# Kernel tuning notes

Hardware: AMD Instinct MI355X
Metric: run time of the kernel (lower is better)

## Reference

```python
import jax, jax.numpy as jnp
import numpy as np

# Config matching init_kwargs: input_shape=(C,T,H,W)=(512,32,14,14), window_size=9, n_heads=8
B, C, T, H, W = 2, 512, 32, 14, 14
N, K = 8, 9
CI = C // N              # per-head inter channels (64)
P = (K - 1) // 2         # symmetric temporal zero-pad so S == T


def setup_inputs() -> dict:
    key = jax.random.key(0)
    ks = jax.random.split(key, 7)
    s = 0.02
    return {
        "x":  jax.random.normal(ks[0], (B, C, T, H, W), jnp.float32),
        # per-head 1x1x1 conv (Linear3d) weights/biases, stacked over heads
        "Wq": jax.random.normal(ks[1], (N, CI, C), jnp.float32) * s,
        "bq": jax.random.normal(ks[2], (N, CI), jnp.float32) * s,
        "Wk": jax.random.normal(ks[3], (N, CI, C), jnp.float32) * s,
        "bk": jax.random.normal(ks[4], (N, CI), jnp.float32) * s,
        "Wv": jax.random.normal(ks[5], (N, CI, C), jnp.float32) * s,
        "bv": jax.random.normal(ks[6], (N, CI), jnp.float32) * s,
    }


def reference(x, Wq, bq, Wk, bk, Wv, bv):
    # x: (B, C, T, H, W). Dropout (p=0.25) is inference-mode identity.
    Bx, Cx, Tx, Hx, Wd = x.shape
    HW = Hx * Wd
    xf = x.reshape(Bx, Cx, Tx, HW)

    # Queries: every original frame is the center of its own window -> project x directly.
    q = jnp.einsum('bctp,nic->bnitp', xf, Wq) + bq[None, :, :, None, None]  # (B,N,ci,T,HW)

    # Keys/values on temporally zero-padded input (Pad3d gives S == T windows).
    xp = jnp.pad(xf, ((0, 0), (0, 0), (P, P), (0, 0)))  # (B,C,T+K-1,HW)
    k = jnp.einsum('bctp,nic->bnitp', xp, Wk) + bk[None, :, :, None, None]
    v = jnp.einsum('bctp,nic->bnitp', xp, Wv) + bv[None, :, :, None, None]

    # Sliding windows over padded time: window s covers padded frames s..s+K-1
    win = jnp.arange(Tx)[:, None] + jnp.arange(K)[None, :]  # (T,K)
    kw = k[:, :, :, win]  # (B,N,ci,T,K,HW)
    vw = v[:, :, :, win].reshape(Bx, N, CI, Tx, K * HW)

    # alpha[b,n,t,p,m] = sum_i q[b,n,i,t,p] * k_win[b,n,i,t,m]; softmax over keys m
    alpha = jnp.einsum('bnitp,bnitkm->bntpkm', q, kw).reshape(Bx, N, Tx, HW, K * HW)
    alpha = jax.nn.softmax(alpha, axis=-1)

    # y = alpha @ value -> (B,N,ci,T,HW); head concat is channel-major reshape
    y = jnp.einsum('bntpm,bnitm->bnitp', alpha, vw)
    z = y.reshape(Bx, Cx, Tx, Hx, Wd) + x  # residual
    return z
```

## Files before the change

### kernel.cpp

```cpp
#include <hip/hip_runtime.h>
#include <hip/hip_bf16.h>
#include <stdint.h>
#include <cstddef>

#define BB  2
#define CC  512
#define TT  32
#define HWP 196
#define NH  8
#define KWIN 9
#define CID 64
#define PPAD 4
#define TP  40
#define MTOT 12544
#define NTOT 1536
#define VSLOT 224
#define LOG2E 1.44269504f

typedef unsigned short u16;
typedef unsigned int   u32;
typedef __attribute__((ext_vector_type(8))) short short8;
typedef __attribute__((ext_vector_type(4))) float floatx4;

__device__ __forceinline__ u16 f2bf(float f) {
    u32 u = __float_as_uint(f);
    u32 r = (u + 0x7fffu + ((u >> 16) & 1u)) >> 16;
    return (u16)r;
}
__device__ __forceinline__ u32 pack2bf(float a, float b) {
    return (u32)f2bf(a) | ((u32)f2bf(b) << 16);
}
__device__ __forceinline__ u32 packtrunc(float a, float b) {
    return __builtin_amdgcn_perm(__float_as_uint(b), __float_as_uint(a), 0x07060302u);
}
__device__ __forceinline__ float fexp2(float x) {
    return __builtin_amdgcn_exp2f(x);
}
__device__ __forceinline__ void gload16(const u16* g, u16* l) {
    __builtin_amdgcn_global_load_lds(
        (const __attribute__((address_space(1))) u32*)g,
        (__attribute__((address_space(3))) u32*)l, 16, 0, 0);
}

__global__ __launch_bounds__(256) void prep_transpose(
    const float* __restrict__ x, u16* __restrict__ xt,
    const float* __restrict__ Wq, const float* __restrict__ Wk,
    const float* __restrict__ Wv, u16* __restrict__ Wbf,
    const float* __restrict__ bk, const float* __restrict__ bv,
    u16* __restrict__ Kout, u16* __restrict__ Vtp)
{
    __shared__ float T[64 * 197];
    int bxg = blockIdx.x;
    int tid = threadIdx.x;

    if (bxg < BB * TT * 8) {
        int bx = bxg;
        int ct = bx & 7; bx >>= 3;
        int t = bx & 31;
        int b = bx >> 5;
        const float* src = x + ((size_t)(b * CC + ct * 64) * TT + t) * HWP;
        for (int i = tid; i < 64 * 49; i += 256) {
            int c = i / 49;
            int p4 = i - c * 49;
            float4 v = *(const float4*)(src + (size_t)c * (TT * HWP) + p4 * 4);
            float* Tp = &T[c * 197 + p4 * 4];
            Tp[0] = v.x; Tp[1] = v.y; Tp[2] = v.z; Tp[3] = v.w;
        }
        __syncthreads();
        u16* dst = xt + (size_t)((b * TT + t) * HWP) * CC + ct * 64;
        for (int i = tid; i < HWP * 8; i += 256) {
            int p = i >> 3;
            int c0 = (i & 7) * 8;
            u32 w[4];
            #pragma unroll
            for (int k = 0; k < 4; k++)
                w[k] = pack2bf(T[(c0 + 2 * k) * 197 + p],
                               T[(c0 + 2 * k + 1) * 197 + p]);
            *(uint4*)(dst + (size_t)p * CC + c0) = *(uint4*)w;
        }
        return;
    }

    int id = (bxg - BB * TT * 8) * 256 + tid;
    const int wtot = NTOT * CC / 2;
    const int kper = 2 * NH * 8 * HWP * 32;
    const int vper = 2 * NH * 8 * 64 * (VSLOT/2);
    if (id < wtot) {
        int c2 = id & 255;
        int oc = id >> 8;
        int kind = oc >> 9;
        int idx = oc & 511;
        const float* src = (kind == 0 ? Wq : (kind == 1 ? Wk : Wv)) + (size_t)idx * CC + c2 * 2;
        ((u32*)Wbf)[id] = pack2bf(src[0], src[1]);
    } else if (id < wtot + kper) {
        int i = id - wtot;
        int ci2 = i & 31; i >>= 5;
        int p = i % HWP;  i /= HWP;
        int fr = i & 7;   i >>= 3;
        int head = i & 7;
        int b = i >> 3;
        int tp = fr < 4 ? fr : fr + 32;
        const float* bias = bk + head * CID + ci2 * 2;
        size_t addr = (((size_t)(b * NH + head) * TP + tp) * HWP + p) * 32 + ci2;
        ((u32*)Kout)[addr] = pack2bf(bias[0], bias[1]);
    } else if (id < wtot + kper + vper) {
        int i = id - wtot - kper;
        int s2 = i % (VSLOT/2); i /= (VSLOT/2);
        int ci = i & 63; i >>= 6;
        int fr = i & 7;  i >>= 3;
        int head = i & 7;
        int b = i >> 3;
        int tp = fr < 4 ? fr : fr + 32;
        float bias = bv[head * CID + ci];
        size_t addr = (((size_t)(b * NH + head) * TP + tp) * 64 + ci) * (VSLOT/2) + s2;
        ((u32*)Vtp)[addr] = pack2bf(bias, bias);
    }
}

__global__ __launch_bounds__(512) void proj_gemm2(
    const u16* __restrict__ xt, const u16* __restrict__ Wbf,
    const float* __restrict__ bq, const float* __restrict__ bk,
    const float* __restrict__ bv,
    u16* __restrict__ Qout, u16* __restrict__ Kout, u16* __restrict__ Vtp)
{
    __shared__ u16 sA[128 * 64];
    __shared__ u16 sB[256 * 64];

    int bx = blockIdx.x;
    int nb = bx % 6;
    int mt = bx / 6;
    int tid = threadIdx.x;
    int wave = tid >> 6, lane = tid & 63, quad = lane >> 4, l15 = lane & 15;
    int wm = wave >> 2, wn = wave & 3;
    int mbase = mt * 128 + wm * 64;
    int nbase = nb * 256 + wn * 64;

    int lr = lane >> 3;
    int sw = ((lane & 7) * 8) ^ (lr << 3);

    floatx4 acc[4][4];
    #pragma unroll
    for (int ms = 0; ms < 4; ms++)
        #pragma unroll
        for (int ns = 0; ns < 4; ns++)
            acc[ms][ns] = (floatx4){0.f, 0.f, 0.f, 0.f};

    const u16* abase = xt + (size_t)(mt * 128) * CC;
    const u16* bbase = Wbf + (size_t)(nb * 256) * CC;

    for (int kc = 0; kc < 8; kc++) {
        __syncthreads();
        #pragma unroll
        for (int i = 0; i < 2; i++) {
            int rbase = wave * 16 + i * 8;
            gload16(abase + (size_t)(rbase + lr) * CC + kc * 64 + sw,
                    &sA[rbase * 64]);
        }
        #pragma unroll
        for (int i = 0; i < 4; i++) {
            int rbase = wave * 32 + i * 8;
            gload16(bbase + (size_t)(rbase + lr) * CC + kc * 64 + sw,
                    &sB[rbase * 64]);
        }
        __syncthreads();

        #pragma unroll
        for (int kk = 0; kk < 2; kk++) {
            int swr = (kk * 32 + quad * 8) ^ ((l15 & 7) << 3);
            short8 af[4], bf[4];
            #pragma unroll
            for (int ms = 0; ms < 4; ms++)
                af[ms] = *(const short8*)&sA[(wm * 64 + ms * 16 + l15) * 64 + swr];
            #pragma unroll
            for (int ns = 0; ns < 4; ns++)
                bf[ns] = *(const short8*)&sB[(wn * 64 + ns * 16 + l15) * 64 + swr];
            #pragma unroll
            for (int ms = 0; ms < 4; ms++)
                #pragma unroll
                for (int ns = 0; ns < 4; ns++)
                    acc[ms][ns] = __builtin_amdgcn_mfma_f32_16x16x32_bf16(
                        af[ms], bf[ns], acc[ms][ns], 0, 0, 0);
        }
    }

    float biasv[4];
    #pragma unroll
    for (int ns = 0; ns < 4; ns++) {
        int n = nbase + ns * 16 + l15;
        int kind = n >> 9;
        int idx = n & 511;
        const float* bpb = kind == 0 ? bq : (kind == 1 ? bk : bv);
        biasv[ns] = bpb[idx];
    }

    #pragma unroll
    for (int ms = 0; ms < 4; ms++) {
        #pragma unroll
        for (int r = 0; r < 4; r++) {
            int m = mbase + ms * 16 + quad * 4 + r;
            int b = m / (TT * HWP);
            int rem = m - b * (TT * HWP);
            int t = rem / HWP;
            int p = rem - t * HWP;
            int slot_p = (p & ~31) | (p & 3) | (((p >> 4) & 1) << 2)
                       | (((p >> 2) & 1) << 3) | (((p >> 3) & 1) << 4);
            #pragma unroll
            for (int ns = 0; ns < 4; ns++) {
                int n = nbase + ns * 16 + l15;
                int kind = n >> 9;
                int idx = n & 511;
                int head = idx >> 6;
                int ci = idx & 63;
                float val = acc[ms][ns][r] + biasv[ns];
                if (kind == 0) {
                    Qout[(((size_t)(b * NH + head) * TT + t) * HWP + p) * CID + ci]
                        = f2bf(val * LOG2E);
                } else if (kind == 1) {
                    Kout[(((size_t)(b * NH + head) * TP + (t + PPAD)) * HWP + p) * CID + ci]
                        = f2bf(val);
                } else {
                    Vtp[(((size_t)(b * NH + head) * TP + (t + PPAD)) * 64 + ci) * VSLOT + slot_p]
                        = f2bf(val);
                }
            }
        }
    }
}

__global__ __launch_bounds__(256, 1) void attn_mfma4(
    const float* __restrict__ x,
    const u16* __restrict__ Qb, const u16* __restrict__ Kb,
    const u16* __restrict__ Vtp, float* __restrict__ zout)
{
    __shared__ float eT[192 * 66];
    __shared__ float eT12[4][4][66];
    __shared__ float ls12[4][4];

    int i = blockIdx.x;
    int xcd = i & 7;
    int r = i >> 3;
    int slab = ((r >= 32) ? 8 : 0) | xcd;
    int t = r & 31;
    int b = slab >> 3, n = slab & 7;

    int tid = threadIdx.x;
    int wave = tid >> 6;
    int lane = tid & 63;
    int quad = lane >> 4, l15 = lane & 15;

    const u16* kfr0 = Kb + (size_t)slab * (TP * HWP) * CID;
    const u16* vslab = Vtp + (size_t)slab * (TP * 64 * VSLOT);
    const float tmask = (quad == 0) ? 1.0f : 0.0f;

    short8 qf[3][2];
    #pragma unroll
    for (int j = 0; j < 3; j++) {
        int qrow = (wave + 4 * j) * 16 + l15;
        const u16* qp = Qb + ((size_t)(slab * TT + t) * HWP + qrow) * CID;
        qf[j][0] = *(const short8*)(qp + quad * 8);
        qf[j][1] = *(const short8*)(qp + 32 + quad * 8);
    }
    short8 qf12[2];
    {
        int qrow = 192 + l15;
        qrow = qrow < HWP ? qrow : (HWP - 1);
        const u16* qp = Qb + ((size_t)(slab * TT + t) * HWP + qrow) * CID;
        qf12[0] = *(const short8*)(qp + quad * 8);
        qf12[1] = *(const short8*)(qp + 32 + quad * 8);
    }

    floatx4 acc[3][4];
    floatx4 accl[3];
    floatx4 acc12[4];
    floatx4 accl12;
    #pragma unroll
    for (int j = 0; j < 3; j++) {
        #pragma unroll
        for (int cg = 0; cg < 4; cg++) acc[j][cg] = (floatx4){0.f, 0.f, 0.f, 0.f};
        accl[j] = (floatx4){0.f, 0.f, 0.f, 0.f};
    }
    #pragma unroll
    for (int cg = 0; cg < 4; cg++) acc12[cg] = (floatx4){0.f, 0.f, 0.f, 0.f};
    accl12 = (floatx4){0.f, 0.f, 0.f, 0.f};

    union { u32 w[4]; short8 s; } ones;
    ones.w[0] = 0x3F803F80u; ones.w[1] = 0x3F803F80u;
    ones.w[2] = 0x3F803F80u; ones.w[3] = 0x3F803F80u;

    #define KLOAD(c, D00, D01, D10, D11) do {                                    \
        const u16* a0_ = kfr0 + (size_t)(rbase + (c) * 32 + l15) * CID + quad * 8;\
        const u16* a1_ = a0_ + (size_t)16 * CID;                                 \
        D00 = *(const short8*)a0_;  D01 = *(const short8*)(a0_ + 32);            \
        D10 = *(const short8*)a1_;  D11 = *(const short8*)(a1_ + 32);            \
    } while (0)

    #define KLOADTAIL(D00, D01) do {                                             \
        int g_ = rbase + 192 + l15;                                              \
        g_ = g_ < (TP * HWP - 1) ? g_ : (TP * HWP - 1);                          \
        const u16* a0_ = kfr0 + (size_t)g_ * CID + quad * 8;                     \
        D00 = *(const short8*)a0_;  D01 = *(const short8*)(a0_ + 32);            \
    } while (0)

    #define VLOAD(c, D0, D1, D2, D3) do {                                        \
        const u16* v_ = vfr + l15 * VSLOT + (c) * 32 + quad * 8;                 \
        D0 = *(const short8*)v_;                                                 \
        D1 = *(const short8*)(v_ + 16 * VSLOT);                                  \
        D2 = *(const short8*)(v_ + 32 * VSLOT);                                  \
        D3 = *(const short8*)(v_ + 48 * VSLOT);                                  \
    } while (0)

    #define CHUNK_ONE(Q0, Q1, ACC, ACCL, K00, K01, K10, K11, V0, V1, V2, V3) do {\
        floatx4 sc0 = (floatx4){0.f, 0.f, 0.f, 0.f};                             \
        sc0 = __builtin_amdgcn_mfma_f32_16x16x32_bf16(K00, Q0, sc0, 0, 0, 0);    \
        sc0 = __builtin_amdgcn_mfma_f32_16x16x32_bf16(K01, Q1, sc0, 0, 0, 0);    \
        floatx4 sc1 = (floatx4){0.f, 0.f, 0.f, 0.f};                             \
        sc1 = __builtin_amdgcn_mfma_f32_16x16x32_bf16(K10, Q0, sc1, 0, 0, 0);    \
        sc1 = __builtin_amdgcn_mfma_f32_16x16x32_bf16(K11, Q1, sc1, 0, 0, 0);    \
        union { u32 w[4]; short8 s; } pf;                                        \
        pf.w[0] = packtrunc(fexp2(sc0[0]), fexp2(sc0[1]));                       \
        pf.w[1] = packtrunc(fexp2(sc0[2]), fexp2(sc0[3]));                       \
        pf.w[2] = packtrunc(fexp2(sc1[0]), fexp2(sc1[1]));                       \
        pf.w[3] = packtrunc(fexp2(sc1[2]), fexp2(sc1[3]));                       \
        ACC[0] = __builtin_amdgcn_mfma_f32_16x16x32_bf16(pf.s, V0, ACC[0], 0, 0, 0); \
        ACC[1] = __builtin_amdgcn_mfma_f32_16x16x32_bf16(pf.s, V1, ACC[1], 0, 0, 0); \
        ACC[2] = __builtin_amdgcn_mfma_f32_16x16x32_bf16(pf.s, V2, ACC[2], 0, 0, 0); \
        ACC[3] = __builtin_amdgcn_mfma_f32_16x16x32_bf16(pf.s, V3, ACC[3], 0, 0, 0); \
        ACCL   = __builtin_amdgcn_mfma_f32_16x16x32_bf16(pf.s, ones.s, ACCL, 0, 0, 0); \
    } while (0)

    #define TAIL_ONE(Q0, Q1, ACC, ACCL, K00, K01, V0, V1, V2, V3) do {           \
        floatx4 sc0 = (floatx4){0.f, 0.f, 0.f, 0.f};                             \
        sc0 = __builtin_amdgcn_mfma_f32_16x16x32_bf16(K00, Q0, sc0, 0, 0, 0);    \
        sc0 = __builtin_amdgcn_mfma_f32_16x16x32_bf16(K01, Q1, sc0, 0, 0, 0);    \
        union { u32 w[4]; short8 s; } pf;                                        \
        pf.w[0] = packtrunc(fexp2(sc0[0]) * tmask, fexp2(sc0[1]) * tmask);       \
        pf.w[1] = packtrunc(fexp2(sc0[2]) * tmask, fexp2(sc0[3]) * tmask);       \
        pf.w[2] = 0u;                                                            \
        pf.w[3] = 0u;                                                            \
        ACC[0] = __builtin_amdgcn_mfma_f32_16x16x32_bf16(pf.s, V0, ACC[0], 0, 0, 0); \
        ACC[1] = __builtin_amdgcn_mfma_f32_16x16x32_bf16(pf.s, V1, ACC[1], 0, 0, 0); \
        ACC[2] = __builtin_amdgcn_mfma_f32_16x16x32_bf16(pf.s, V2, ACC[2], 0, 0, 0); \
        ACC[3] = __builtin_amdgcn_mfma_f32_16x16x32_bf16(pf.s, V3, ACC[3], 0, 0, 0); \
        ACCL   = __builtin_amdgcn_mfma_f32_16x16x32_bf16(pf.s, ones.s, ACCL, 0, 0, 0); \
    } while (0)

    #define CHUNK_FULL(K00, K01, K10, K11, V0, V1, V2, V3) do {                  \
        _Pragma("unroll")                                                        \
        for (int j = 0; j < 3; j++)                                              \
            CHUNK_ONE(qf[j][0], qf[j][1], acc[j], accl[j],                       \
                      K00, K01, K10, K11, V0, V1, V2, V3);                       \
        if (do12)                                                                \
            CHUNK_ONE(qf12[0], qf12[1], acc12, accl12,                           \
                      K00, K01, K10, K11, V0, V1, V2, V3);                       \
    } while (0)

    #define CHUNK_TAIL(K00, K01, V0, V1, V2, V3) do {                            \
        _Pragma("unroll")                                                        \
        for (int j = 0; j < 3; j++)                                              \
            TAIL_ONE(qf[j][0], qf[j][1], acc[j], accl[j],                        \
                     K00, K01, V0, V1, V2, V3);                                  \
        if (do12)                                                                \
            TAIL_ONE(qf12[0], qf12[1], acc12, accl12,                            \
                     K00, K01, V0, V1, V2, V3);                                  \
    } while (0)

    for (int f = 0; f < KWIN; f++) {
        int rbase = (t + f) * HWP;
        const u16* vfr = vslab + (size_t)(t + f) * (64 * VSLOT);
        bool do12 = ((f & 3) == wave);

        short8 ka00, ka01, ka10, ka11, va0, va1, va2, va3;
        short8 kb00, kb01, kb10, kb11, vb0, vb1, vb2, vb3;
        short8 kc00, kc01, kc10, kc11, vc0, vc1, vc2, vc3;

        KLOAD(0, ka00, ka01, ka10, ka11);  VLOAD(0, va0, va1, va2, va3);
        KLOAD(1, kb00, kb01, kb10, kb11);  VLOAD(1, vb0, vb1, vb2, vb3);
        KLOAD(2, kc00, kc01, kc10, kc11);  VLOAD(2, vc0, vc1, vc2, vc3);
        CHUNK_FULL(ka00, ka01, ka10, ka11, va0, va1, va2, va3);
        KLOAD(3, ka00, ka01, ka10, ka11);  VLOAD(3, va0, va1, va2, va3);
        CHUNK_FULL(kb00, kb01, kb10, kb11, vb0, vb1, vb2, vb3);
        KLOAD(4, kb00, kb01, kb10, kb11);  VLOAD(4, vb0, vb1, vb2, vb3);
        CHUNK_FULL(kc00, kc01, kc10, kc11, vc0, vc1, vc2, vc3);
        KLOAD(5, kc00, kc01, kc10, kc11);  VLOAD(5, vc0, vc1, vc2, vc3);
        CHUNK_FULL(ka00, ka01, ka10, ka11, va0, va1, va2, va3);
        KLOADTAIL(ka00, ka01);             VLOAD(6, va0, va1, va2, va3);
        CHUNK_FULL(kb00, kb01, kb10, kb11, vb0, vb1, vb2, vb3);
        CHUNK_FULL(kc00, kc01, kc10, kc11, vc0, vc1, vc2, vc3);
        CHUNK_TAIL(ka00, ka01, va0, va1, va2, va3);
    }

    #undef KLOAD
    #undef KLOADTAIL
    #undef VLOAD
    #undef CHUNK_ONE
    #undef TAIL_ONE
    #undef CHUNK_FULL
    #undef CHUNK_TAIL

    #pragma unroll
    for (int j = 0; j < 3; j++) {
        int tg = wave + 4 * j;
        float il[4];
        #pragma unroll
        for (int rr = 0; rr < 4; rr++) il[rr] = 1.0f / accl[j][rr];
        #pragma unroll
        for (int cg = 0; cg < 4; cg++) {
            #pragma unroll
            for (int rr = 0; rr < 4; rr++) {
                int p = tg * 16 + quad * 4 + rr;
                eT[p * 66 + cg * 16 + l15] = acc[j][cg][rr] * il[rr];
            }
        }
    }
    if (quad == 0) {
        #pragma unroll
        for (int rr = 0; rr < 4; rr++) {
            #pragma unroll
            for (int cg = 0; cg < 4; cg++)
                eT12[wave][rr][cg * 16 + l15] = acc12[cg][rr];
            if (l15 == 0) ls12[wave][rr] = accl12[rr];
        }
    }
    __syncthreads();

    if (tid < HWP) {
        size_t base = ((size_t)(b * CC + n * CID) * TT + t) * HWP + tid;
        if (tid < 192) {
            for (int ci = 0; ci < 64; ci++) {
                size_t a = base + (size_t)ci * (TT * HWP);
                zout[a] = eT[tid * 66 + ci] + x[a];
            }
        } else {
            int rr = tid - 192;
            float l = ls12[0][rr] + ls12[1][rr] + ls12[2][rr] + ls12[3][rr];
            float il = 1.0f / l;
            for (int ci = 0; ci < 64; ci++) {
                size_t a = base + (size_t)ci * (TT * HWP);
                float v = (eT12[0][rr][ci] + eT12[1][rr][ci]
                         + eT12[2][rr][ci] + eT12[3][rr][ci]) * il;
                zout[a] = v + x[a];
            }
        }
    }
}

extern "C" void kernel_launch(void* const* d_in, const int* in_sizes, int n_in,
                              void* d_out, int out_size, void* d_ws, size_t ws_size,
                              hipStream_t stream) {
    const float* x  = (const float*)d_in[0];
    const float* Wq = (const float*)d_in[1];
    const float* bq = (const float*)d_in[2];
    const float* Wk = (const float*)d_in[3];
    const float* bk = (const float*)d_in[4];
    const float* Wv = (const float*)d_in[5];
    const float* bv = (const float*)d_in[6];
    float* z = (float*)d_out;

    const size_t qElems   = (size_t)BB * NH * TT * HWP * CID;
    const size_t kElems   = (size_t)BB * NH * TP * HWP * CID;
    const size_t vtpElems = (size_t)BB * NH * TP * 64 * VSLOT;

    u16* Qw  = (u16*)d_ws;
    u16* Kw  = Qw + qElems;
    u16* Vtp = Kw + kElems;
    u16* Wb  = Vtp + vtpElems;
    u16* Xt  = (u16*)d_out;

    {
        const int wtot = NTOT * CC / 2;
        const int kper = 2 * NH * 8 * HWP * 32;
        const int vper = 2 * NH * 8 * 64 * (VSLOT / 2);
        const int prepBlocks = (wtot + kper + vper + 255) / 256;
        prep_transpose<<<BB * TT * 8 + prepBlocks, 256, 0, stream>>>(
            x, Xt, Wq, Wk, Wv, Wb, bk, bv, Kw, Vtp);
    }
    proj_gemm2<<<98 * 6, 512, 0, stream>>>(Xt, Wb, bq, bk, bv, Qw, Kw, Vtp);
    attn_mfma4<<<512, 256, 0, stream>>>(x, Qw, Kw, Vtp, z);
}
```

Measured before the change: 239.3 us.

## Stage K/V frames in swizzled shared memory instead of per-wave global loads

Each key frame's K and V tiles are now copied cooperatively into LDS, with an XOR swizzle on K, using gload16 before the chunk loop. The MFMA fragments are then read from LDS rather than fetched redundantly from global memory by every wave. The LDS is unioned with the epilogue buffers. This adds two block-wide barriers per frame and removes the register-level software pipelining of global loads, so the copies are no longer overlapped with compute.

```diff
diff --git a/kernel.cpp b/kernel.cpp
--- a/kernel.cpp
+++ b/kernel.cpp
@@ -232,9 +232,10 @@
     const u16* __restrict__ Qb, const u16* __restrict__ Kb,
     const u16* __restrict__ Vtp, float* __restrict__ zout)
 {
-    __shared__ float eT[192 * 66];
-    __shared__ float eT12[4][4][66];
-    __shared__ float ls12[4][4];
+    __shared__ union {
+        struct { u16 K[26 * 512]; u16 V[28 * 512]; } s;
+        struct { float eT[192 * 66]; float eT12[4][4][66]; float ls12[4][4]; } e;
+    } u;
 
     int i = blockIdx.x;
     int xcd = i & 7;
@@ -247,6 +248,8 @@
     int wave = tid >> 6;
     int lane = tid & 63;
     int quad = lane >> 4, l15 = lane & 15;
+    int lr = lane >> 3;
+    int ksw = ((lane & 7) * 8) ^ (lr << 3);
 
     const u16* kfr0 = Kb + (size_t)slab * (TP * HWP) * CID;
     const u16* vslab = Vtp + (size_t)slab * (TP * 64 * VSLOT);
@@ -287,23 +290,28 @@
     ones.w[0] = 0x3F803F80u; ones.w[1] = 0x3F803F80u;
     ones.w[2] = 0x3F803F80u; ones.w[3] = 0x3F803F80u;
 
-    #define KLOAD(c, D00, D01, D10, D11) do {                                    \
-        const u16* a0_ = kfr0 + (size_t)(rbase + (c) * 32 + l15) * CID + quad * 8;\
-        const u16* a1_ = a0_ + (size_t)16 * CID;                                 \
-        D00 = *(const short8*)a0_;  D01 = *(const short8*)(a0_ + 32);            \
-        D10 = *(const short8*)a1_;  D11 = *(const short8*)(a1_ + 32);            \
-    } while (0)
-
-    #define KLOADTAIL(D00, D01) do {                                             \
-        int g_ = rbase + 192 + l15;                                              \
-        g_ = g_ < (TP * HWP - 1) ? g_ : (TP * HWP - 1);                          \
-        const u16* a0_ = kfr0 + (size_t)g_ * CID + quad * 8;                     \
-        D00 = *(const short8*)a0_;  D01 = *(const short8*)(a0_ + 32);            \
-    } while (0)
-
-    #define VLOAD(c, D0, D1, D2, D3) do {                                        \
-        const u16* v_ = vfr + l15 * VSLOT + (c) * 32 + quad * 8;                 \
-        D0 = *(const short8*)v_;                                                 \
+    #define KLOAD_L(c, D00, D01, D10, D11) do {                                  \
+        int r0_ = (c) * 32 + l15;                                                \
+        int sx_ = (l15 & 7) << 3;                                                \
+        const u16* a0_ = &u.s.K[r0_ * 64];                                       \
+        const u16* a1_ = &u.s.K[(r0_ + 16) * 64];                                \
+        D00 = *(const short8*)(a0_ + ((quad * 8) ^ sx_));                        \
+        D01 = *(const short8*)(a0_ + ((32 + quad * 8) ^ sx_));                   \
+        D10 = *(const short8*)(a1_ + ((quad * 8) ^ sx_));                        \
+        D11 = *(const short8*)(a1_ + ((32 + quad * 8) ^ sx_));                   \
+    } while (0)
+
+    #define KLOADTAIL_L(D00, D01) do {                                           \
+        int r0_ = 192 + l15;                                                     \
+        int sx_ = (l15 & 7) << 3;                                                \
+        const u16* a0_ = &u.s.K[r0_ * 64];                                       \
+        D00 = *(const short8*)(a0_ + ((quad * 8) ^ sx_));                        \
+        D01 = *(const short8*)(a0_ + ((32 + quad * 8) ^ sx_));                   \
+    } while (0)
+
+    #define VLOAD_L(c, D0, D1, D2, D3) do {                                      \
+        const u16* v_ = &u.s.V[l15 * VSLOT + (c) * 32 + quad * 8];               \
+        D0 = *(const short8*)(v_);                                               \
         D1 = *(const short8*)(v_ + 16 * VSLOT);                                  \
         D2 = *(const short8*)(v_ + 32 * VSLOT);                                  \
         D3 = *(const short8*)(v_ + 48 * VSLOT);                                  \
@@ -366,37 +374,49 @@
 
     for (int f = 0; f < KWIN; f++) {
         int rbase = (t + f) * HWP;
+        const u16* kfr = kfr0 + (size_t)rbase * CID;
         const u16* vfr = vslab + (size_t)(t + f) * (64 * VSLOT);
         bool do12 = ((f & 3) == wave);
 
-        short8 ka00, ka01, ka10, ka11, va0, va1, va2, va3;
-        short8 kb00, kb01, kb10, kb11, vb0, vb1, vb2, vb3;
-        short8 kc00, kc01, kc10, kc11, vc0, vc1, vc2, vc3;
-
-        KLOAD(0, ka00, ka01, ka10, ka11);  VLOAD(0, va0, va1, va2, va3);
-        KLOAD(1, kb00, kb01, kb10, kb11);  VLOAD(1, vb0, vb1, vb2, vb3);
-        KLOAD(2, kc00, kc01, kc10, kc11);  VLOAD(2, vc0, vc1, vc2, vc3);
-        CHUNK_FULL(ka00, ka01, ka10, ka11, va0, va1, va2, va3);
-        KLOAD(3, ka00, ka01, ka10, ka11);  VLOAD(3, va0, va1, va2, va3);
-        CHUNK_FULL(kb00, kb01, kb10, kb11, vb0, vb1, vb2, vb3);
-        KLOAD(4, kb00, kb01, kb10, kb11);  VLOAD(4, vb0, vb1, vb2, vb3);
-        CHUNK_FULL(kc00, kc01, kc10, kc11, vc0, vc1, vc2, vc3);
-        KLOAD(5, kc00, kc01, kc10, kc11);  VLOAD(5, vc0, vc1, vc2, vc3);
-        CHUNK_FULL(ka00, ka01, ka10, ka11, va0, va1, va2, va3);
-        KLOADTAIL(ka00, ka01);             VLOAD(6, va0, va1, va2, va3);
-        CHUNK_FULL(kb00, kb01, kb10, kb11, vb0, vb1, vb2, vb3);
-        CHUNK_FULL(kc00, kc01, kc10, kc11, vc0, vc1, vc2, vc3);
-        CHUNK_TAIL(ka00, ka01, va0, va1, va2, va3);
-    }
-
-    #undef KLOAD
-    #undef KLOADTAIL
-    #undef VLOAD
+        __syncthreads();
+        #pragma unroll
+        for (int it = 0; it < 14; it++) {
+            int idx = it * 4 + wave;
+            if (idx < 26) {
+                gload16(kfr + (size_t)(idx * 8 + lr) * CID + ksw,
+                        &u.s.K[idx * 512]);
+            } else if (idx < 54) {
+                int j2 = idx - 26;
+                gload16(vfr + j2 * 512 + lane * 8, &u.s.V[j2 * 512]);
+            }
+        }
+        __syncthreads();
+
+        #pragma unroll
+        for (int c = 0; c < 6; c++) {
+            short8 k00, k01, k10, k11, v0, v1, v2, v3;
+            KLOAD_L(c, k00, k01, k10, k11);
+            VLOAD_L(c, v0, v1, v2, v3);
+            CHUNK_FULL(k00, k01, k10, k11, v0, v1, v2, v3);
+        }
+        {
+            short8 k00, k01, v0, v1, v2, v3;
+            KLOADTAIL_L(k00, k01);
+            VLOAD_L(6, v0, v1, v2, v3);
+            CHUNK_TAIL(k00, k01, v0, v1, v2, v3);
+        }
+    }
+
+    #undef KLOAD_L
+    #undef KLOADTAIL_L
+    #undef VLOAD_L
     #undef CHUNK_ONE
     #undef TAIL_ONE
     #undef CHUNK_FULL
     #undef CHUNK_TAIL
 
+    __syncthreads();
+
     #pragma unroll
     for (int j = 0; j < 3; j++) {
         int tg = wave + 4 * j;
@@ -408,7 +428,7 @@
             #pragma unroll
             for (int rr = 0; rr < 4; rr++) {
                 int p = tg * 16 + quad * 4 + rr;
-                eT[p * 66 + cg * 16 + l15] = acc[j][cg][rr] * il[rr];
+                u.e.eT[p * 66 + cg * 16 + l15] = acc[j][cg][rr] * il[rr];
             }
         }
     }
@@ -417,8 +437,8 @@
         for (int rr = 0; rr < 4; rr++) {
             #pragma unroll
             for (int cg = 0; cg < 4; cg++)
-                eT12[wave][rr][cg * 16 + l15] = acc12[cg][rr];
-            if (l15 == 0) ls12[wave][rr] = accl12[rr];
+                u.e.eT12[wave][rr][cg * 16 + l15] = acc12[cg][rr];
+            if (l15 == 0) u.e.ls12[wave][rr] = accl12[rr];
         }
     }
     __syncthreads();
@@ -428,16 +448,17 @@
         if (tid < 192) {
             for (int ci = 0; ci < 64; ci++) {
                 size_t a = base + (size_t)ci * (TT * HWP);
-                zout[a] = eT[tid * 66 + ci] + x[a];
+                zout[a] = u.e.eT[tid * 66 + ci] + x[a];
             }
         } else {
             int rr = tid - 192;
-            float l = ls12[0][rr] + ls12[1][rr] + ls12[2][rr] + ls12[3][rr];
+            float l = u.e.ls12[0][rr] + u.e.ls12[1][rr]
+                    + u.e.ls12[2][rr] + u.e.ls12[3][rr];
             float il = 1.0f / l;
             for (int ci = 0; ci < 64; ci++) {
                 size_t a = base + (size_t)ci * (TT * HWP);
-                float v = (eT12[0][rr][ci] + eT12[1][rr][ci]
-                         + eT12[2][rr][ci] + eT12[3][rr][ci]) * il;
+                float v = (u.e.eT12[0][rr][ci] + u.e.eT12[1][rr][ci]
+                         + u.e.eT12[2][rr][ci] + u.e.eT12[3][rr][ci]) * il;
                 zout[a] = v + x[a];
             }
         }
```

Measured after the change: 213.0 us. 11.0% less time.
